# Kernel tuning notes

Measured on AMD Instinct MI355X. Metric: run time of the kernel, lower is better.

Reference implementation:

```python
import jax, jax.numpy as jnp
import numpy as np

N_NODES = 100000
N_EDGES = 1600000
DIMS = [64, 64, 64, 32]  # in -> hid -> hid -> out


def setup_inputs() -> dict:
    key = jax.random.key(0)
    ks = jax.random.split(key, 12)
    features = jax.random.normal(ks[0], (N_NODES, DIMS[0]), dtype=jnp.float32)
    edge_weights = jax.random.uniform(ks[1], (N_EDGES,), dtype=jnp.float32)
    src = jax.random.randint(ks[2], (N_EDGES,), 0, N_NODES, dtype=jnp.int32)
    dst = jax.random.randint(ks[3], (N_EDGES,), 0, N_NODES, dtype=jnp.int32)
    def lin(kw, kb, i, o):
        s = 1.0 / np.sqrt(i)
        W = jax.random.uniform(kw, (i, o), minval=-s, maxval=s, dtype=jnp.float32)
        b = jax.random.uniform(kb, (o,), minval=-s, maxval=s, dtype=jnp.float32)
        return W, b
    W1, b1 = lin(ks[4], ks[5], DIMS[0], DIMS[1])
    W2, b2 = lin(ks[6], ks[7], DIMS[1], DIMS[2])
    Wp, bp = lin(ks[8], ks[9], DIMS[2], DIMS[3])
    return {"features": features, "edge_weights": edge_weights, "src": src,
            "dst": dst, "W1": W1, "b1": b1, "W2": W2, "b2": b2,
            "Wp": Wp, "bp": bp}


def _graph_conv(x, src, dst, ew, W, b, norm_src, norm_dst):
    # DGL GraphConv, norm='both', with edge weights:
    # h = D_in^{-1/2} * A_w * (D_out^{-1/2} * x) @ W + b
    h = x * norm_src[:, None]
    msg = h[src] * ew[:, None]                      # [E, d] gather + edge-weight
    agg = jax.ops.segment_sum(msg, dst, num_segments=N_NODES)  # scatter-sum
    agg = agg * norm_dst[:, None]
    return agg @ W + b


def reference(features, edge_weights, src, dst, W1, b1, W2, b2, Wp, bp):
    ones = jnp.ones((N_EDGES,), dtype=features.dtype)
    out_deg = jax.ops.segment_sum(ones, src, num_segments=N_NODES)
    in_deg = jax.ops.segment_sum(ones, dst, num_segments=N_NODES)
    norm_src = jnp.power(jnp.clip(out_deg, 1.0, None), -0.5)
    norm_dst = jnp.power(jnp.clip(in_deg, 1.0, None), -0.5)

    x = jax.nn.relu(_graph_conv(features, src, dst, edge_weights, W1, b1, norm_src, norm_dst))
    x = jax.nn.relu(_graph_conv(x, src, dst, edge_weights, W2, b2, norm_src, norm_dst))
    x = _graph_conv(x, src, dst, edge_weights, Wp, bp, norm_src, norm_dst)
    return x
```

## Files before the change

### kernel.cpp

```cpp
#include <hip/hip_runtime.h>

#define N_NODES 100000
#define N_EDGES 1600000
#define NB_SCAN 391
#define NSLICE 64
#define SLICE_E 25000
#define NBUCK 4
#define BUCK_N 25000
#define BUCK_W 12500

__device__ __forceinline__ unsigned short f2bf(float f) {
    unsigned int u = __float_as_uint(f);
    return (unsigned short)((u + 0x7FFFu + ((u >> 16) & 1u)) >> 16);
}


template <bool RANK>
__global__ void __launch_bounds__(512) count_kernel(
        const int* __restrict__ ids,
        unsigned short* __restrict__ slicecnt,
        unsigned short* __restrict__ rank16) {
    __shared__ unsigned int cnt[BUCK_W];
    int s = blockIdx.x >> 2;
    int b = blockIdx.x & 3;
    int b0 = b * BUCK_N;
    for (int w = threadIdx.x; w < BUCK_W; w += 512) cnt[w] = 0;
    __syncthreads();
    int base = s * SLICE_E;
    for (int i = threadIdx.x; i < SLICE_E; i += 512) {
        int e = base + i;
        int id = ids[e] - b0;
        if ((unsigned)id < (unsigned)BUCK_N) {
            unsigned int shift = (id & 1) * 16;
            unsigned int old = atomicAdd(&cnt[id >> 1], 1u << shift);
            if (RANK) rank16[e] = (unsigned short)((old >> shift) & 0xFFFFu);
        }
    }
    __syncthreads();
    unsigned int* row = (unsigned int*)(slicecnt + (size_t)s * N_NODES) + b * BUCK_W;
    for (int w = threadIdx.x; w < BUCK_W; w += 512) row[w] = cnt[w];
}

__global__ void scan_slices_kernel(unsigned short* __restrict__ scd,
                                   const unsigned short* __restrict__ scs,
                                   int* __restrict__ deg_int,
                                   float* __restrict__ ndq,
                                   float* __restrict__ norm_src,
                                   int* __restrict__ block_sums) {
    __shared__ int sdata[256];
    int t = threadIdx.x;
    int n = blockIdx.x * blockDim.x + t;
    int deg = 0;
    if (n < N_NODES) {
        unsigned int tot = 0;
        for (int s = 0; s < NSLICE; ++s) {
            size_t idx = (size_t)s * N_NODES + n;
            unsigned int c = scd[idx];
            scd[idx] = (unsigned short)tot;
            tot += c;
        }
        deg = (int)tot;
        deg_int[n] = deg;
        ndq[n] = rsqrtf(fmaxf((float)tot, 1.0f)) * (1.0f / 32767.0f);
        unsigned int so = 0;
        for (int s = 0; s < NSLICE; ++s) so += scs[(size_t)s * N_NODES + n];
        norm_src[n] = rsqrtf(fmaxf((float)so, 1.0f));
    }
    sdata[t] = deg;
    __syncthreads();
    for (int off = 128; off > 0; off >>= 1) {
        if (t < off) sdata[t] += sdata[t + off];
        __syncthreads();
    }
    if (t == 0) block_sums[blockIdx.x] = sdata[0];
}


__global__ void scan_blocks_kernel(const int* __restrict__ block_sums, int* __restrict__ block_off) {
    __shared__ int part[512];
    int t = threadIdx.x;
    int v = (t < NB_SCAN) ? block_sums[t] : 0;
    part[t] = v;
    __syncthreads();
    for (int off = 1; off < 512; off <<= 1) {
        int u = (t >= off) ? part[t - off] : 0;
        __syncthreads();
        part[t] += u;
        __syncthreads();
    }
    if (t < NB_SCAN) block_off[t] = part[t] - v;
}

__global__ void scatter_rowptr_kernel(const int* __restrict__ deg_in,
                                      const int* __restrict__ block_off,
                                      int* __restrict__ row_ptr) {
    __shared__ int part[256];
    int t = threadIdx.x;
    int n = blockIdx.x * 256 + t;
    int v = (n < N_NODES) ? deg_in[n] : 0;
    part[t] = v;
    __syncthreads();
    for (int off = 1; off < 256; off <<= 1) {
        int u = (t >= off) ? part[t - off] : 0;
        __syncthreads();
        part[t] += u;
        __syncthreads();
    }
    int excl = part[t] - v + block_off[blockIdx.x];
    if (n < N_NODES) row_ptr[n] = excl;
    if (n == N_NODES - 1) row_ptr[N_NODES] = excl + v;
}


__global__ void fill_kernel(const int* __restrict__ src, const int* __restrict__ dst,
                            const float* __restrict__ ew,
                            const int* __restrict__ row_ptr,
                            const unsigned short* __restrict__ sliceoff,
                            const unsigned short* __restrict__ rank16,
                            unsigned int* __restrict__ epack) {
    int i = blockIdx.x * blockDim.x + threadIdx.x;
    int stride = gridDim.x * blockDim.x;
    for (int e = i; e < N_EDGES; e += stride) {
        int s = src[e], d = dst[e];
        int sl = e / SLICE_E;
        int slot = row_ptr[d] + (int)sliceoff[(size_t)sl * N_NODES + d] + (int)rank16[e];
        unsigned int q = (unsigned int)(ew[e] * 32767.0f + 0.5f);
        epack[slot] = ((unsigned int)s << 15) | q;
    }
}


template <int BM, int DOUT, bool BIAS_RELU>
__global__ void __launch_bounds__(256) matmul_kernel(
        const float* __restrict__ x, const float* __restrict__ W,
        const float* __restrict__ bin, const float* __restrict__ ns,
        unsigned short* __restrict__ h) {
    constexpr int S = 65;
    constexpr int CG = DOUT / 4;
    __shared__ float Xs[BM * S];
    __shared__ float Ws[64 * DOUT];
    int tid = threadIdx.x;
    int n0 = blockIdx.x * BM;

    for (int i = tid; i < 16 * DOUT; i += 256)
        ((float4*)Ws)[i] = ((const float4*)W)[i];

    float4 bv4;
    if (BIAS_RELU) bv4 = ((const float4*)bin)[tid & 15];
    int c0 = (tid & 15) * 4;
    for (int r = tid >> 4; r < BM; r += 16) {
        int n = n0 + r;
        int nc = n < N_NODES ? n : N_NODES - 1;
        float4 v = ((const float4*)(x + (size_t)nc * 64))[tid & 15];
        if (BIAS_RELU) {
            v.x = fmaxf(v.x + bv4.x, 0.0f);
            v.y = fmaxf(v.y + bv4.y, 0.0f);
            v.z = fmaxf(v.z + bv4.z, 0.0f);
            v.w = fmaxf(v.w + bv4.w, 0.0f);
        }
        Xs[r * S + c0]     = v.x;
        Xs[r * S + c0 + 1] = v.y;
        Xs[r * S + c0 + 2] = v.z;
        Xs[r * S + c0 + 3] = v.w;
    }
    __syncthreads();

    int cg = tid % CG;
    int ng = tid / CG;
    float acc[4][4];
#pragma unroll
    for (int i = 0; i < 4; ++i)
#pragma unroll
        for (int j = 0; j < 4; ++j) acc[i][j] = 0.0f;

#pragma unroll 16
    for (int k = 0; k < 64; ++k) {
        float4 wk = *(const float4*)(&Ws[k * DOUT + cg * 4]);
        float xk[4];
#pragma unroll
        for (int i = 0; i < 4; ++i) xk[i] = Xs[(ng * 4 + i) * S + k];
#pragma unroll
        for (int i = 0; i < 4; ++i) {
            acc[i][0] = fmaf(xk[i], wk.x, acc[i][0]);
            acc[i][1] = fmaf(xk[i], wk.y, acc[i][1]);
            acc[i][2] = fmaf(xk[i], wk.z, acc[i][2]);
            acc[i][3] = fmaf(xk[i], wk.w, acc[i][3]);
        }
    }

#pragma unroll
    for (int i = 0; i < 4; ++i) {
        int n = n0 + ng * 4 + i;
        if (n < N_NODES) {
            float nsv = ns[n];
            ushort4 o;
            o.x = f2bf(acc[i][0] * nsv); o.y = f2bf(acc[i][1] * nsv);
            o.z = f2bf(acc[i][2] * nsv); o.w = f2bf(acc[i][3] * nsv);
            *(ushort4*)(&h[(size_t)n * DOUT + cg * 4]) = o;
        }
    }
}


template <int D, bool FINAL>
__global__ void __launch_bounds__(256) csr_agg_kernel(
        const int* __restrict__ row_ptr,
        const unsigned int* __restrict__ epack,
        const unsigned short* __restrict__ h,
        const float* __restrict__ ndq,
        const float* __restrict__ bias, float* __restrict__ out) {
    constexpr int G = D / 2;
    constexpr int EPL = 64 / G;
    int tid = blockIdx.x * blockDim.x + threadIdx.x;
    int wave = tid >> 6;
    int nwaves = (gridDim.x * blockDim.x) >> 6;
    int lane = threadIdx.x & 63;
    int grp = lane / G;
    int j = lane % G;
    int l16 = lane & 15;
    const unsigned int* hw = (const unsigned int*)h;

    float bx = 0.f, by = 0.f;
    if (FINAL) { bx = bias[2 * j]; by = bias[2 * j + 1]; }

    for (int n = wave; n < N_NODES; n += nwaves) {
        int s = row_ptr[n];
        int e = row_ptr[n + 1];
        float ax[4] = {0.f, 0.f, 0.f, 0.f};
        float ay[4] = {0.f, 0.f, 0.f, 0.f};
        for (int base = s; base < e; base += 16) {
            int idx = base + l16;
            unsigned int pk = (idx < e) ? epack[idx] : 0u;
#pragma unroll
            for (int i = 0; i < 16; i += EPL) {
                constexpr int KM = 4 - 1;
                int k = i / EPL;
                unsigned int p = __shfl(pk, i + grp);
                unsigned int hv = hw[(size_t)(p >> 15) * G + j];
                float c = (float)(p & 32767u);
                ax[k & KM] = fmaf(__uint_as_float(hv << 16), c, ax[k & KM]);
                ay[k & KM] = fmaf(__uint_as_float(hv & 0xFFFF0000u), c, ay[k & KM]);
            }
        }
        float sx = (ax[0] + ax[1]) + (ax[2] + ax[3]);
        float sy = (ay[0] + ay[1]) + (ay[2] + ay[3]);
        if (EPL == 4) {
            sx += __shfl(sx, lane ^ 16);
            sy += __shfl(sy, lane ^ 16);
        }
        sx += __shfl(sx, lane ^ 32);
        sy += __shfl(sy, lane ^ 32);
        if (grp == 0) {
            float nv = ndq[n];
            float2 o;
            o.x = fmaf(sx, nv, bx);
            o.y = fmaf(sy, nv, by);
            *(float2*)(&out[(size_t)n * D + 2 * j]) = o;
        }
    }
}

extern "C" void kernel_launch(void* const* d_in, const int* in_sizes, int n_in,
                              void* d_out, int out_size, void* d_ws, size_t ws_size,
                              hipStream_t stream) {
    const float* features = (const float*)d_in[0];
    const float* ew       = (const float*)d_in[1];
    const int*   src      = (const int*)d_in[2];
    const int*   dst      = (const int*)d_in[3];
    const float* W1       = (const float*)d_in[4];
    const float* b1       = (const float*)d_in[5];
    const float* W2       = (const float*)d_in[6];
    const float* b2       = (const float*)d_in[7];
    const float* Wp       = (const float*)d_in[8];
    const float* bp       = (const float*)d_in[9];
    float* out = (float*)d_out;

    float* ws = (float*)d_ws;
    float* norm_src = ws;
    float* ndq      = ws + 100000;
    int*   deg_int  = (int*)(ws + 200000);
    int*   row_ptr  = (int*)(ws + 300000);
    int*   block_sums = (int*)(ws + 400002);
    int*   block_off  = (int*)(ws + 400394);
    unsigned short* rank16 = (unsigned short*)(ws + 400800);
    unsigned int*   epack  = (unsigned int*)(ws + 1200800);
    unsigned short* hbuf   = (unsigned short*)(ws + 2800800);
    float*          bufA   = ws + 6000800;

    unsigned short* slicecnt_dst = hbuf;
    unsigned short* slicecnt_src = (unsigned short*)bufA;

    count_kernel<true><<<NSLICE * NBUCK, 512, 0, stream>>>(dst, slicecnt_dst, rank16);
    count_kernel<false><<<NSLICE * NBUCK, 512, 0, stream>>>(src, slicecnt_src, nullptr);
    scan_slices_kernel<<<NB_SCAN, 256, 0, stream>>>(slicecnt_dst, slicecnt_src,
                                                    deg_int, ndq, norm_src, block_sums);
    scan_blocks_kernel<<<1, 512, 0, stream>>>(block_sums, block_off);
    scatter_rowptr_kernel<<<NB_SCAN, 256, 0, stream>>>(deg_int, block_off, row_ptr);
    fill_kernel<<<2048, 256, 0, stream>>>(src, dst, ew, row_ptr,
                                          slicecnt_dst, rank16, epack);

    matmul_kernel<64, 64, false><<<1563, 256, 0, stream>>>(features, W1, nullptr, norm_src, hbuf);
    csr_agg_kernel<64, false><<<8192, 256, 0, stream>>>(row_ptr, epack, hbuf, ndq, nullptr, bufA);

    matmul_kernel<64, 64, true><<<1563, 256, 0, stream>>>(bufA, W2, b1, norm_src, hbuf);
    csr_agg_kernel<64, false><<<8192, 256, 0, stream>>>(row_ptr, epack, hbuf, ndq, nullptr, bufA);

    matmul_kernel<128, 32, true><<<782, 256, 0, stream>>>(bufA, Wp, b2, norm_src, hbuf);
    csr_agg_kernel<32, true><<<8192, 256, 0, stream>>>(row_ptr, epack, hbuf, ndq, bp, out);
}
```

Before: 258.0 us.

## Build CSR via two-level bucket partition and per-bucket local sort

Replaces the slice-count, multi-kernel scan and rank-based fill CSR construction with a two-pass approach. Edges are first partitioned into 128 destination buckets using shared-memory staging and global atomics. Each bucket is then histogrammed, scanned and scattered within one block, which also emits row_ptr and the dst norm. This is meant to cut global passes and launch count. The risks are a fixed per-bucket capacity (SCAP), which silently drops edges if a bucket overflows, and non-deterministic edge order within rows.

Result: slower. 272.1 us (+5.5%).

```diff
diff --git a/kernel.cpp b/kernel.cpp
--- a/kernel.cpp
+++ b/kernel.cpp
@@ -9,17 +9,21 @@
 #define BUCK_N 25000
 #define BUCK_W 12500
 
+#define NBUCK2 128
+#define BUCK2_N 782
+#define SCAP 14000
+#define CHUNK 4096
+#define ACAP 64
+
 __device__ __forceinline__ unsigned short f2bf(float f) {
     unsigned int u = __float_as_uint(f);
     return (unsigned short)((u + 0x7FFFu + ((u >> 16) & 1u)) >> 16);
 }
 
 
-template <bool RANK>
-__global__ void __launch_bounds__(512) count_kernel(
+__global__ void __launch_bounds__(512) count_src_kernel(
         const int* __restrict__ ids,
-        unsigned short* __restrict__ slicecnt,
-        unsigned short* __restrict__ rank16) {
+        unsigned short* __restrict__ slicecnt) {
     __shared__ unsigned int cnt[BUCK_W];
     int s = blockIdx.x >> 2;
     int b = blockIdx.x & 3;
@@ -28,104 +32,159 @@
     __syncthreads();
     int base = s * SLICE_E;
     for (int i = threadIdx.x; i < SLICE_E; i += 512) {
-        int e = base + i;
-        int id = ids[e] - b0;
-        if ((unsigned)id < (unsigned)BUCK_N) {
-            unsigned int shift = (id & 1) * 16;
-            unsigned int old = atomicAdd(&cnt[id >> 1], 1u << shift);
-            if (RANK) rank16[e] = (unsigned short)((old >> shift) & 0xFFFFu);
-        }
+        int id = ids[base + i] - b0;
+        if ((unsigned)id < (unsigned)BUCK_N)
+            atomicAdd(&cnt[id >> 1], 1u << ((id & 1) * 16));
     }
     __syncthreads();
     unsigned int* row = (unsigned int*)(slicecnt + (size_t)s * N_NODES) + b * BUCK_W;
     for (int w = threadIdx.x; w < BUCK_W; w += 512) row[w] = cnt[w];
 }
 
-__global__ void scan_slices_kernel(unsigned short* __restrict__ scd,
-                                   const unsigned short* __restrict__ scs,
-                                   int* __restrict__ deg_int,
-                                   float* __restrict__ ndq,
-                                   float* __restrict__ norm_src,
-                                   int* __restrict__ block_sums) {
-    __shared__ int sdata[256];
+__global__ void norm_src_kernel(const unsigned short* __restrict__ scs,
+                                float* __restrict__ norm_src) {
+    int n = blockIdx.x * blockDim.x + threadIdx.x;
+    if (n >= N_NODES) return;
+    unsigned int so = 0;
+    for (int s = 0; s < NSLICE; ++s) so += scs[(size_t)s * N_NODES + n];
+    norm_src[n] = rsqrtf(fmaxf((float)so, 1.0f));
+}
+
+
+__global__ void __launch_bounds__(256) partition_kernel(
+        const int* __restrict__ src, const int* __restrict__ dst,
+        const float* __restrict__ ew,
+        unsigned int* __restrict__ cur,
+        unsigned int* __restrict__ stagedR, unsigned int* __restrict__ stagedD) {
+    __shared__ unsigned int sR[NBUCK2][ACAP];
+    __shared__ unsigned short sD[NBUCK2][ACAP];
+    __shared__ unsigned int lcnt[NBUCK2];
+    __shared__ unsigned int gbase[NBUCK2];
+    int tid = threadIdx.x;
+    for (int b = tid; b < NBUCK2; b += 256) lcnt[b] = 0;
+    __syncthreads();
+    int e0 = blockIdx.x * CHUNK;
+    int ecount = min(CHUNK, N_EDGES - e0);
+    for (int i = tid; i < ecount; i += 256) {
+        int e = e0 + i;
+        int d = dst[e];
+        int s = src[e];
+        unsigned int q = (unsigned int)(ew[e] * 32767.0f + 0.5f);
+        unsigned int rec = ((unsigned int)s << 15) | q;
+        int b = d / BUCK2_N;
+        unsigned int dl = (unsigned int)(d - b * BUCK2_N);
+        unsigned int pos = atomicAdd(&lcnt[b], 1u);
+        if (pos < ACAP) {
+            sR[b][pos] = rec;
+            sD[b][pos] = (unsigned short)dl;
+        } else {
+            unsigned int g = atomicAdd(&cur[b], 1u);
+            if (g < SCAP) {
+                stagedR[(size_t)b * SCAP + g] = rec;
+                stagedD[(size_t)b * SCAP + g] = dl;
+            }
+        }
+    }
+    __syncthreads();
+    for (int b = tid; b < NBUCK2; b += 256)
+        gbase[b] = atomicAdd(&cur[b], min(lcnt[b], (unsigned)ACAP));
+    __syncthreads();
+    int wid = tid >> 6, lane = tid & 63;
+    for (int b = wid; b < NBUCK2; b += 4) {
+        unsigned int c = min(lcnt[b], (unsigned)ACAP);
+        unsigned int gb = gbase[b];
+        for (unsigned int k = lane; k < c; k += 64) {
+            stagedR[(size_t)b * SCAP + gb + k] = sR[b][k];
+            stagedD[(size_t)b * SCAP + gb + k] = sD[b][k];
+        }
+    }
+}
+
+__global__ void bucket_scan_kernel(const unsigned int* __restrict__ cur,
+                                   unsigned int* __restrict__ bucket_base) {
+    __shared__ unsigned int p[NBUCK2];
     int t = threadIdx.x;
-    int n = blockIdx.x * blockDim.x + t;
-    int deg = 0;
-    if (n < N_NODES) {
-        unsigned int tot = 0;
-        for (int s = 0; s < NSLICE; ++s) {
-            size_t idx = (size_t)s * N_NODES + n;
-            unsigned int c = scd[idx];
-            scd[idx] = (unsigned short)tot;
-            tot += c;
-        }
-        deg = (int)tot;
-        deg_int[n] = deg;
-        ndq[n] = rsqrtf(fmaxf((float)tot, 1.0f)) * (1.0f / 32767.0f);
-        unsigned int so = 0;
-        for (int s = 0; s < NSLICE; ++s) so += scs[(size_t)s * N_NODES + n];
-        norm_src[n] = rsqrtf(fmaxf((float)so, 1.0f));
-    }
-    sdata[t] = deg;
-    __syncthreads();
-    for (int off = 128; off > 0; off >>= 1) {
-        if (t < off) sdata[t] += sdata[t + off];
+    unsigned int v = min(cur[t], (unsigned)SCAP);
+    p[t] = v;
+    __syncthreads();
+    for (int off = 1; off < NBUCK2; off <<= 1) {
+        unsigned int u = (t >= off) ? p[t - off] : 0;
         __syncthreads();
-    }
-    if (t == 0) block_sums[blockIdx.x] = sdata[0];
-}
-
-
-__global__ void scan_blocks_kernel(const int* __restrict__ block_sums, int* __restrict__ block_off) {
-    __shared__ int part[512];
+        p[t] += u;
+        __syncthreads();
+    }
+    bucket_base[t] = p[t] - v;
+    if (t == NBUCK2 - 1) bucket_base[NBUCK2] = p[t];
+}
+
+
+__global__ void __launch_bounds__(512) sort_build_kernel(
+        const unsigned int* __restrict__ cur,
+        const unsigned int* __restrict__ bucket_base,
+        const unsigned int* __restrict__ stagedR,
+        const unsigned int* __restrict__ stagedD,
+        unsigned int* __restrict__ epack,
+        int* __restrict__ row_ptr, float* __restrict__ ndq) {
+    __shared__ unsigned int hist[BUCK2_N];
+    __shared__ unsigned int cur2[BUCK2_N];
+    __shared__ unsigned int part[512];
+    int b = blockIdx.x;
     int t = threadIdx.x;
-    int v = (t < NB_SCAN) ? block_sums[t] : 0;
-    part[t] = v;
+    unsigned int m = min(cur[b], (unsigned)SCAP);
+    unsigned int base = bucket_base[b];
+    const unsigned int* sR = stagedR + (size_t)b * SCAP;
+    const unsigned int* sD = stagedD + (size_t)b * SCAP;
+
+    for (int i = t; i < BUCK2_N; i += 512) hist[i] = 0;
+    __syncthreads();
+    for (unsigned int i = t; i < m; i += 512) atomicAdd(&hist[sD[i]], 1u);
+    __syncthreads();
+
+    unsigned int deg0 = 0, deg1 = 0, loc0 = 0, loc1 = 0, sum = 0;
+    {
+        int i0 = t * 2, i1 = t * 2 + 1;
+        deg0 = (i0 < BUCK2_N) ? hist[i0] : 0;
+        deg1 = (i1 < BUCK2_N) ? hist[i1] : 0;
+        loc0 = 0; loc1 = deg0; sum = deg0 + deg1;
+    }
+    part[t] = sum;
     __syncthreads();
     for (int off = 1; off < 512; off <<= 1) {
-        int u = (t >= off) ? part[t - off] : 0;
+        unsigned int u = (t >= off) ? part[t - off] : 0;
         __syncthreads();
         part[t] += u;
         __syncthreads();
     }
-    if (t < NB_SCAN) block_off[t] = part[t] - v;
-}
-
-__global__ void scatter_rowptr_kernel(const int* __restrict__ deg_in,
-                                      const int* __restrict__ block_off,
-                                      int* __restrict__ row_ptr) {
-    __shared__ int part[256];
-    int t = threadIdx.x;
-    int n = blockIdx.x * 256 + t;
-    int v = (n < N_NODES) ? deg_in[n] : 0;
-    part[t] = v;
-    __syncthreads();
-    for (int off = 1; off < 256; off <<= 1) {
-        int u = (t >= off) ? part[t - off] : 0;
-        __syncthreads();
-        part[t] += u;
-        __syncthreads();
-    }
-    int excl = part[t] - v + block_off[blockIdx.x];
-    if (n < N_NODES) row_ptr[n] = excl;
-    if (n == N_NODES - 1) row_ptr[N_NODES] = excl + v;
-}
-
-
-__global__ void fill_kernel(const int* __restrict__ src, const int* __restrict__ dst,
-                            const float* __restrict__ ew,
-                            const int* __restrict__ row_ptr,
-                            const unsigned short* __restrict__ sliceoff,
-                            const unsigned short* __restrict__ rank16,
-                            unsigned int* __restrict__ epack) {
-    int i = blockIdx.x * blockDim.x + threadIdx.x;
-    int stride = gridDim.x * blockDim.x;
-    for (int e = i; e < N_EDGES; e += stride) {
-        int s = src[e], d = dst[e];
-        int sl = e / SLICE_E;
-        int slot = row_ptr[d] + (int)sliceoff[(size_t)sl * N_NODES + d] + (int)rank16[e];
-        unsigned int q = (unsigned int)(ew[e] * 32767.0f + 0.5f);
-        epack[slot] = ((unsigned int)s << 15) | q;
+    unsigned int pre = (t == 0) ? 0 : part[t - 1];
+    __syncthreads();
+    {
+        int i0 = t * 2, i1 = t * 2 + 1;
+        if (i0 < BUCK2_N) {
+            unsigned int off0 = pre + loc0;
+            cur2[i0] = off0;
+            int n = b * BUCK2_N + i0;
+            if (n < N_NODES) {
+                row_ptr[n] = (int)(base + off0);
+                ndq[n] = rsqrtf(fmaxf((float)deg0, 1.0f)) * (1.0f / 32767.0f);
+            }
+        }
+        if (i1 < BUCK2_N) {
+            unsigned int off1 = pre + loc1;
+            cur2[i1] = off1;
+            int n = b * BUCK2_N + i1;
+            if (n < N_NODES) {
+                row_ptr[n] = (int)(base + off1);
+                ndq[n] = rsqrtf(fmaxf((float)deg1, 1.0f)) * (1.0f / 32767.0f);
+            }
+        }
+    }
+    if (b == NBUCK2 - 1 && t == 0) row_ptr[N_NODES] = (int)(base + m);
+    __syncthreads();
+
+    for (unsigned int i = t; i < m; i += 512) {
+        unsigned int rec = sR[i];
+        unsigned int r = atomicAdd(&cur2[sD[i]], 1u);
+        epack[base + r] = rec;
     }
 }
 
@@ -276,28 +335,27 @@
     float* out = (float*)d_out;
 
     float* ws = (float*)d_ws;
-    float* norm_src = ws;
-    float* ndq      = ws + 100000;
-    int*   deg_int  = (int*)(ws + 200000);
-    int*   row_ptr  = (int*)(ws + 300000);
-    int*   block_sums = (int*)(ws + 400002);
-    int*   block_off  = (int*)(ws + 400394);
-    unsigned short* rank16 = (unsigned short*)(ws + 400800);
-    unsigned int*   epack  = (unsigned int*)(ws + 1200800);
-    unsigned short* hbuf   = (unsigned short*)(ws + 2800800);
-    float*          bufA   = ws + 6000800;
-
-    unsigned short* slicecnt_dst = hbuf;
+    float*        norm_src    = ws;
+    float*        ndq         = ws + 100000;
+    int*          row_ptr     = (int*)(ws + 200000);
+    unsigned int* cur         = (unsigned int*)(ws + 300002);
+    unsigned int* bucket_base = (unsigned int*)(ws + 300130);
+    unsigned int* epack       = (unsigned int*)(ws + 300260);
+    unsigned int* stagedR     = (unsigned int*)(ws + 1900260);
+    unsigned int* stagedD     = (unsigned int*)(ws + 3692260);
+    unsigned short* hbuf      = (unsigned short*)(ws + 1900260);
+    float*        bufA        = ws + 5484260;
     unsigned short* slicecnt_src = (unsigned short*)bufA;
 
-    count_kernel<true><<<NSLICE * NBUCK, 512, 0, stream>>>(dst, slicecnt_dst, rank16);
-    count_kernel<false><<<NSLICE * NBUCK, 512, 0, stream>>>(src, slicecnt_src, nullptr);
-    scan_slices_kernel<<<NB_SCAN, 256, 0, stream>>>(slicecnt_dst, slicecnt_src,
-                                                    deg_int, ndq, norm_src, block_sums);
-    scan_blocks_kernel<<<1, 512, 0, stream>>>(block_sums, block_off);
-    scatter_rowptr_kernel<<<NB_SCAN, 256, 0, stream>>>(deg_int, block_off, row_ptr);
-    fill_kernel<<<2048, 256, 0, stream>>>(src, dst, ew, row_ptr,
-                                          slicecnt_dst, rank16, epack);
+    hipMemsetAsync(cur, 0, NBUCK2 * sizeof(unsigned int), stream);
+    partition_kernel<<<(N_EDGES + CHUNK - 1) / CHUNK, 256, 0, stream>>>(
+        src, dst, ew, cur, stagedR, stagedD);
+    bucket_scan_kernel<<<1, NBUCK2, 0, stream>>>(cur, bucket_base);
+    sort_build_kernel<<<NBUCK2, 512, 0, stream>>>(cur, bucket_base, stagedR, stagedD,
+                                                  epack, row_ptr, ndq);
+
+    count_src_kernel<<<NSLICE * NBUCK, 512, 0, stream>>>(src, slicecnt_src);
+    norm_src_kernel<<<NB_SCAN, 256, 0, stream>>>(slicecnt_src, norm_src);
 
     matmul_kernel<64, 64, false><<<1563, 256, 0, stream>>>(features, W1, nullptr, norm_src, hbuf);
     csr_agg_kernel<64, false><<<8192, 256, 0, stream>>>(row_ptr, epack, hbuf, ndq, nullptr, bufA);
```
